# Performance work log

Hardware: AMD Instinct MI355X
Metric: run time of the kernel (lower is better)

The kernel has to match this reference:

```python
import jax, jax.numpy as jnp
import numpy as np

B, C, H, W = 2, 256, 64, 64  # C = in_channels; x has 2*C channels
DQ = C // 16


def setup_inputs() -> dict:
    key = jax.random.key(0)
    ks = jax.random.split(key, 10)
    s = 0.05
    return {
        "x": jax.random.normal(ks[0], (B, 2 * C, H, W), dtype=jnp.float32),
        "Wq": jax.random.normal(ks[1], (DQ, C), dtype=jnp.float32) * s,
        "bq": jax.random.normal(ks[2], (DQ,), dtype=jnp.float32) * s,
        "Wk": jax.random.normal(ks[3], (DQ, C), dtype=jnp.float32) * s,
        "bk": jax.random.normal(ks[4], (DQ,), dtype=jnp.float32) * s,
        "Wv": jax.random.normal(ks[5], (C, C), dtype=jnp.float32) * s,
        "bv": jax.random.normal(ks[6], (C,), dtype=jnp.float32) * s,
        "Wpt": jax.random.normal(ks[7], (C, 2 * C), dtype=jnp.float32) * s,
        "bpt": jax.random.normal(ks[8], (C,), dtype=jnp.float32) * s,
        "gamma": jnp.full((1,), 0.5, dtype=jnp.float32),  # original inits to 0; nonzero for a non-trivial output
    }


def _conv1x1(x, Wt, b):
    # 1x1 conv == per-pixel linear map over channels
    return jnp.einsum("bchw,dc->bdhw", x, Wt) + b[None, :, None, None]


def reference(x, Wq, bq, Wk, bk, Wv, bv, Wpt, bpt, gamma):
    n = x.shape[1] // 2
    x1, x2 = x[:, :n], x[:, n:]
    b, c, h, w = x1.shape
    hw = h * w

    def qkv(xi):
        q = _conv1x1(xi, Wq, bq).reshape(b, DQ, hw)   # [B,dq,HW]
        k = _conv1x1(xi, Wk, bk).reshape(b, DQ, hw)   # [B,dq,HW]
        v = _conv1x1(xi, Wv, bv).reshape(b, c, hw)    # [B,C,HW]
        return q, k, v

    q1, k1, v1 = qkv(x1)
    q2, k2, v2 = qkv(x2)

    # attn[b,i,j] = softmax_j( q[:,i] . k[:,j] )  (no scaling, as in original)
    attn1 = jax.nn.softmax(jnp.einsum("bdi,bdj->bij", q1, k1), axis=-1)  # [B,HW,HW]
    attn2 = jax.nn.softmax(jnp.einsum("bdi,bdj->bij", q2, k2), axis=-1)

    def apply_attn(v, attn):
        # out[b,c,i] = sum_j v[b,c,j] * attn[b,i,j]
        return jnp.einsum("bcj,bij->bci", v, attn).reshape(b, c, h, w)

    out11 = apply_attn(v1, attn1)
    out12 = apply_attn(v2, attn1)
    out21 = apply_attn(v1, attn2)
    out22 = apply_attn(v2, attn2)

    o1 = _conv1x1(jnp.concatenate([out11, out12], axis=1), Wpt, bpt)  # [B,C,H,W]
    o2 = _conv1x1(jnp.concatenate([out21, out22], axis=1), Wpt, bpt)

    out = gamma * jnp.concatenate([o1, o2], axis=1) + x
    return out
```

## Files before the change

### kernel.cpp

```cpp
#include <hip/hip_runtime.h>
#include <hip/hip_bf16.h>


#define HW 4096
#define CC 256
#define DQ 16

typedef __hip_bfloat16 bf16;
struct alignas(8) bh4 { bf16 x, y, z, w; };
typedef __bf16 bf16x8 __attribute__((ext_vector_type(8)));
typedef float  f32x4  __attribute__((ext_vector_type(4)));

static __device__ __forceinline__ float b2f(bf16 v) { return __bfloat162float(v); }

static __device__ __forceinline__ void load_lds16(const void* g, void* l) {
    __builtin_amdgcn_global_load_lds(
        (const __attribute__((address_space(1))) unsigned int*)g,
        (__attribute__((address_space(3))) unsigned int*)l, 16, 0, 0);
}

static __device__ __forceinline__ bf16x8 ones8() {
    union { unsigned int u[4]; bf16x8 v; } t;
    t.u[0] = t.u[1] = t.u[2] = t.u[3] = 0x3F803F80u;
    return t.v;
}

struct ConvArgs { const void* src[9]; float* dst[9]; int n[9]; };
__global__ void convert_weights(ConvArgs a, const unsigned short* __restrict__ probe) {
    int seg = blockIdx.y;
    int i = blockIdx.x * 256 + threadIdx.x;
    bool isb = probe[0] != 0;
    if (i < a.n[seg])
        a.dst[seg][i] = isb ? b2f(((const bf16*)a.src[seg])[i])
                            : ((const float*)a.src[seg])[i];
}

__global__ void w_to_bf16(const float* __restrict__ Wqf, const float* __restrict__ Wkf,
                          bf16* __restrict__ Wqb, bf16* __restrict__ Wkb) {
    int i = blockIdx.x * 256 + threadIdx.x;
    const float* s = blockIdx.y ? Wkf : Wqf;
    bf16* d = blockIdx.y ? Wkb : Wqb;
    d[i] = __float2bfloat16(s[i]);
}

__global__ void convert_x_t(const void* __restrict__ xsrc, bf16* __restrict__ Xt,
                            const unsigned short* __restrict__ probe) {
    __shared__ float T[64][65];
    int t = threadIdx.x;
    int j0 = blockIdx.x * 64, e0 = blockIdx.y * 64, b = blockIdx.z;
    bool isb = probe[0] != 0;
    int j_l = t & 63, er0 = (t >> 6) * 16;
#pragma unroll
    for (int r = 0; r < 16; ++r) {
        size_t src = ((size_t)(b * 512 + e0 + er0 + r)) * HW + j0 + j_l;
        T[er0 + r][j_l] = isb ? b2f(((const bf16*)xsrc)[src]) : ((const float*)xsrc)[src];
    }
    __syncthreads();
    int e_w = t & 63, jr0 = (t >> 6) * 16;
#pragma unroll
    for (int r = 0; r < 16; ++r)
        Xt[((size_t)b * HW + j0 + jr0 + r) * 512 + e0 + e_w] = __float2bfloat16(T[e_w][jr0 + r]);
}

__global__ void build_mc(const float* __restrict__ Wv, const float* __restrict__ bv,
                         const float* __restrict__ Wpt, const float* __restrict__ bpt,
                         bf16* __restrict__ McB, float* __restrict__ btot) {
    int blk = blockIdx.x, tid = threadIdx.x;
    if (blk < 512) {
        int d = blk >> 1;
        int c = ((blk & 1) << 8) + tid;
        int half = c >> 8, cm = c & 255;
        float acc = 0.f;
        for (int e = 0; e < 256; ++e)
            acc = fmaf(Wpt[d * 512 + half * 256 + e], Wv[e * 256 + cm], acc);
        McB[d * 512 + c] = __float2bfloat16(acc);
    } else {
        int d = tid;
        float acc = bpt[d];
        for (int e = 0; e < 256; ++e)
            acc = fmaf(Wpt[d * 512 + e] + Wpt[d * 512 + 256 + e], bv[e], acc);
        btot[d] = acc;
    }
}

__global__ void __launch_bounds__(256)
build_qk_mfma(const bf16* __restrict__ Xt,
              const bf16* __restrict__ Wqb, const float* __restrict__ bqf,
              const bf16* __restrict__ Wkb, const float* __restrict__ bkf,
              bf16* __restrict__ Qb, bf16* __restrict__ Kb) {
    int tid = threadIdx.x;
    int lane = tid & 63, wave = tid >> 6;
    int ln = lane & 15, q = lane >> 4;
    int bh = blockIdx.y;
    int b = bh >> 1, h = bh & 1;
    int j0 = blockIdx.x * 64 + wave * 16;

    bf16x8 aQ[8], aK[8];
#pragma unroll
    for (int kk = 0; kk < 8; ++kk) {
        aQ[kk] = *(const bf16x8*)&Wqb[ln * 256 + kk * 32 + q * 8];
        aK[kk] = *(const bf16x8*)&Wkb[ln * 256 + kk * 32 + q * 8];
    }
    const bf16* Xrow = Xt + ((size_t)b * HW + j0 + ln) * 512 + h * 256;
    f32x4 dQ = {0.f, 0.f, 0.f, 0.f}, dK = {0.f, 0.f, 0.f, 0.f};
#pragma unroll
    for (int kk = 0; kk < 8; ++kk) {
        bf16x8 bx = *(const bf16x8*)&Xrow[kk * 32 + q * 8];
        dQ = __builtin_amdgcn_mfma_f32_16x16x32_bf16(aQ[kk], bx, dQ, 0, 0, 0);
        dK = __builtin_amdgcn_mfma_f32_16x16x32_bf16(aK[kk], bx, dK, 0, 0, 0);
    }
    size_t rowoff = ((size_t)bh * HW + j0 + ln) * 32;
    bh4 oq, ok;
    oq.x = __float2bfloat16(dQ[0] + bqf[q * 4 + 0]);
    oq.y = __float2bfloat16(dQ[1] + bqf[q * 4 + 1]);
    oq.z = __float2bfloat16(dQ[2] + bqf[q * 4 + 2]);
    oq.w = __float2bfloat16(dQ[3] + bqf[q * 4 + 3]);
    ok.x = __float2bfloat16(dK[0] + bkf[q * 4 + 0]);
    ok.y = __float2bfloat16(dK[1] + bkf[q * 4 + 1]);
    ok.z = __float2bfloat16(dK[2] + bkf[q * 4 + 2]);
    ok.w = __float2bfloat16(dK[3] + bkf[q * 4 + 3]);
    bh4 z; z.x = z.y = z.z = z.w = __float2bfloat16(0.f);
    *(bh4*)&Qb[rowoff + q * 4] = oq;
    *(bh4*)&Qb[rowoff + 16 + q * 4] = z;
    *(bh4*)&Kb[rowoff + q * 4] = ok;
    *(bh4*)&Kb[rowoff + 16 + q * 4] = z;
}

__global__ void __launch_bounds__(256, 2)
build_u_mfma(const bf16* __restrict__ McB, const bf16* __restrict__ Xt,
             bf16* __restrict__ Ub) {
    __shared__ __align__(16) bf16 sA[64 * 64];
    __shared__ __align__(16) bf16 sB[128 * 64];
    int tid = threadIdx.x;
    int lane = tid & 63, wave = tid >> 6;
    int ln = lane & 15, q = lane >> 4;
    int wm = (wave >> 1) * 32, wn = (wave & 1) * 64;
    int j0 = blockIdx.x * 128, c0 = blockIdx.y * 64, b = blockIdx.z;
    const bf16* Xb = Xt + (size_t)b * HW * 512;
    f32x4 acc[2][4];
#pragma unroll
    for (int mi = 0; mi < 2; ++mi)
#pragma unroll
        for (int ni = 0; ni < 4; ++ni)
#pragma unroll
            for (int r = 0; r < 4; ++r) acc[mi][ni][r] = 0.f;

    for (int e0 = 0; e0 < 512; e0 += 64) {
        __syncthreads();
#pragma unroll
        for (int r = 0; r < 2; ++r) {
            int s = r * 256 + tid;
            int row = s >> 3, jc = s & 7, jg = jc ^ (row & 7);
            load_lds16(McB + (size_t)(c0 + row) * 512 + e0 + jg * 8, sA + s * 8);
        }
#pragma unroll
        for (int r = 0; r < 4; ++r) {
            int s = r * 256 + tid;
            int row = s >> 3, jc = s & 7, jg = jc ^ (row & 7);
            load_lds16(Xb + (size_t)(j0 + row) * 512 + e0 + jg * 8, sB + s * 8);
        }
        __syncthreads();
#pragma unroll
        for (int kh = 0; kh < 2; ++kh) {
            bf16x8 af[2], bfv[4];
#pragma unroll
            for (int mi = 0; mi < 2; ++mi) {
                int row = wm + mi * 16 + ln;
                int jc = (kh * 4 + q) ^ (row & 7);
                af[mi] = *(const bf16x8*)&sA[row * 64 + jc * 8];
            }
#pragma unroll
            for (int ni = 0; ni < 4; ++ni) {
                int row = wn + ni * 16 + ln;
                int jc = (kh * 4 + q) ^ (row & 7);
                bfv[ni] = *(const bf16x8*)&sB[row * 64 + jc * 8];
            }
#pragma unroll
            for (int mi = 0; mi < 2; ++mi)
#pragma unroll
                for (int ni = 0; ni < 4; ++ni)
                    acc[mi][ni] = __builtin_amdgcn_mfma_f32_16x16x32_bf16(
                        af[mi], bfv[ni], acc[mi][ni], 0, 0, 0);
        }
    }
#pragma unroll
    for (int mi = 0; mi < 2; ++mi)
#pragma unroll
        for (int r = 0; r < 4; ++r) {
            int c = c0 + wm + mi * 16 + q * 4 + r;
#pragma unroll
            for (int ni = 0; ni < 4; ++ni) {
                int j = j0 + wn + ni * 16 + ln;
                Ub[((size_t)(b * CC + c)) * HW + j] = __float2bfloat16(acc[mi][ni][r]);
            }
        }
}

__global__ void __launch_bounds__(256, 4)
compute_E_mfma(const bf16* __restrict__ Qb, const bf16* __restrict__ Kb,
               bf16* __restrict__ E, long estride, int bh_base) {
    int tid = threadIdx.x;
    int lane = tid & 63, wave = tid >> 6;
    int ln = lane & 15, q = lane >> 4;
    int bh = bh_base + blockIdx.z;
    bf16* Eb = E + (size_t)blockIdx.z * estride;
    int i0 = blockIdx.x * 64 + wave * 16;
    int j0 = blockIdx.y * 1024;
    bf16x8 bq = *(const bf16x8*)&Qb[((size_t)bh * HW + i0 + ln) * 32 + q * 8];
    bf16* erow = Eb + (size_t)(i0 + ln) * HW + q * 4;
    for (int jt = 0; jt < 64; ++jt) {
        int j = j0 + jt * 16;
        bf16x8 ak = *(const bf16x8*)&Kb[((size_t)bh * HW + j + ln) * 32 + q * 8];
        f32x4 d = {0.f, 0.f, 0.f, 0.f};
        d = __builtin_amdgcn_mfma_f32_16x16x32_bf16(ak, bq, d, 0, 0, 0);
        bh4 o;
        o.x = __float2bfloat16(__expf(d[0]));
        o.y = __float2bfloat16(__expf(d[1]));
        o.z = __float2bfloat16(__expf(d[2]));
        o.w = __float2bfloat16(__expf(d[3]));
        *(bh4*)&erow[j] = o;
    }
}

__global__ void __launch_bounds__(256, 2)
attn_mfma(const bf16* __restrict__ Ub, const bf16* __restrict__ E, long estride,
          const float* __restrict__ btot,
          const void* __restrict__ xorig, const float* __restrict__ gamf,
          void* __restrict__ outv, const unsigned short* __restrict__ probe,
          int bh_base) {
    __shared__ __align__(16) bf16 sA[128 * 64];
    __shared__ __align__(16) bf16 sB[64 * 64];
    int tid  = threadIdx.x;
    int lane = tid & 63, wave = tid >> 6;
    int ln = lane & 15, q = lane >> 4;
    int wm = (wave & 1) * 64, wn = (wave >> 1) * 32;
    int i0 = blockIdx.x * 64, c0 = blockIdx.y * 128;
    int bh = bh_base + blockIdx.z;
    int b = bh >> 1, h = bh & 1;
    const bf16* Eb = E + (size_t)blockIdx.z * estride;
    const bf16* Ubb = Ub + (size_t)b * CC * HW;
    const bf16x8 ONE = ones8();

    f32x4 acc[4][2], accS[2];
#pragma unroll
    for (int ni = 0; ni < 2; ++ni) {
#pragma unroll
        for (int r = 0; r < 4; ++r) accS[ni][r] = 0.f;
#pragma unroll
        for (int mi = 0; mi < 4; ++mi)
#pragma unroll
            for (int r = 0; r < 4; ++r) acc[mi][ni][r] = 0.f;
    }

    for (int j0 = 0; j0 < HW; j0 += 64) {
        __syncthreads();
#pragma unroll
        for (int r = 0; r < 4; ++r) {
            int s = r * 256 + tid;
            int row = s >> 3, jc = s & 7, jg = jc ^ (row & 7);
            load_lds16(Ubb + (size_t)(c0 + row) * HW + j0 + jg * 8, sA + s * 8);
        }
#pragma unroll
        for (int r = 0; r < 2; ++r) {
            int s = r * 256 + tid;
            int row = s >> 3, jc = s & 7, jg = jc ^ (row & 7);
            load_lds16(Eb + (size_t)(i0 + row) * HW + j0 + jg * 8, sB + s * 8);
        }
        __syncthreads();
#pragma unroll
        for (int kh = 0; kh < 2; ++kh) {
            bf16x8 af[4], bfv[2];
#pragma unroll
            for (int mi = 0; mi < 4; ++mi) {
                int row = wm + mi * 16 + ln;
                int jc = (kh * 4 + q) ^ (row & 7);
                af[mi] = *(const bf16x8*)&sA[row * 64 + jc * 8];
            }
#pragma unroll
            for (int ni = 0; ni < 2; ++ni) {
                int row = wn + ni * 16 + ln;
                int jc = (kh * 4 + q) ^ (row & 7);
                bfv[ni] = *(const bf16x8*)&sB[row * 64 + jc * 8];
            }
#pragma unroll
            for (int ni = 0; ni < 2; ++ni) {
                accS[ni] = __builtin_amdgcn_mfma_f32_16x16x32_bf16(
                    ONE, bfv[ni], accS[ni], 0, 0, 0);
#pragma unroll
                for (int mi = 0; mi < 4; ++mi)
                    acc[mi][ni] = __builtin_amdgcn_mfma_f32_16x16x32_bf16(
                        af[mi], bfv[ni], acc[mi][ni], 0, 0, 0);
            }
        }
    }

    bool isb = probe[0] != 0;
    float g = gamf[0];
    float lv[2];
#pragma unroll
    for (int ni = 0; ni < 2; ++ni)
        lv[ni] = 1.f / accS[ni][0];
#pragma unroll
    for (int mi = 0; mi < 4; ++mi)
#pragma unroll
        for (int r = 0; r < 4; ++r) {
            int c = c0 + wm + mi * 16 + q * 4 + r;
            float bt = btot[c];
            size_t rowbase = ((size_t)(b * 512 + h * 256 + c)) * HW + i0 + wn;
#pragma unroll
            for (int ni = 0; ni < 2; ++ni) {
                size_t idx = rowbase + ni * 16 + ln;
                float xres = isb ? b2f(((const bf16*)xorig)[idx]) : ((const float*)xorig)[idx];
                float o = fmaf(g, fmaf(acc[mi][ni][r], lv[ni], bt), xres);
                if (isb) ((bf16*)outv)[idx] = __float2bfloat16(o);
                else     ((float*)outv)[idx] = o;
            }
        }
}

extern "C" void kernel_launch(void* const* d_in, const int* in_sizes, int n_in,
                              void* d_out, int out_size, void* d_ws, size_t ws_size,
                              hipStream_t stream) {
    const unsigned short* probe = (const unsigned short*)d_in[9];

    char* ws = (char*)d_ws;
    size_t off = 0;
    auto alloc = [&](size_t bytes) { size_t r = off; off = (off + bytes + 255) & ~(size_t)255; return r; };
    const int wsz[9] = {DQ * 256, DQ, DQ * 256, DQ, 256 * 256, 256, 256 * 512, 256, 1};
    float* wf[9];
    for (int t = 0; t < 9; ++t) wf[t] = (float*)(ws + alloc((size_t)wsz[t] * 4));
    bf16*  Xt   = (bf16*)(ws + alloc((size_t)2 * HW * 512 * 2));
    bf16*  McB  = (bf16*)(ws + alloc(256 * 512 * 2));
    float* btot = (float*)(ws + alloc(256 * 4));
    bf16*  Wqb  = (bf16*)(ws + alloc(DQ * 256 * 2));
    bf16*  Wkb  = (bf16*)(ws + alloc(DQ * 256 * 2));
    bf16*  Qb   = (bf16*)(ws + alloc((size_t)4 * HW * 32 * 2));
    bf16*  Kb   = (bf16*)(ws + alloc((size_t)4 * HW * 32 * 2));
    bf16*  Ub   = (bf16*)(ws + alloc((size_t)2 * CC * HW * 2));
    const size_t ESZ = (size_t)HW * HW * 2;
    bf16* E = (bf16*)(ws + off);
    const long ESTRIDE = (long)HW * HW;
    int NZ = (ws_size >= off + 4 * ESZ) ? 4 : 1;

    ConvArgs ca;
    for (int t = 0; t < 9; ++t) { ca.src[t] = d_in[t + 1]; ca.dst[t] = wf[t]; ca.n[t] = wsz[t]; }
    convert_weights<<<dim3(512, 9), 256, 0, stream>>>(ca, probe);
    w_to_bf16<<<dim3(16, 2), 256, 0, stream>>>(wf[0], wf[2], Wqb, Wkb);
    convert_x_t<<<dim3(64, 8, 2), 256, 0, stream>>>(d_in[0], Xt, probe);

    build_mc<<<513, 256, 0, stream>>>(wf[4], wf[5], wf[6], wf[7], McB, btot);
    build_qk_mfma<<<dim3(64, 4), 256, 0, stream>>>(Xt, Wqb, wf[1], Wkb, wf[3], Qb, Kb);
    build_u_mfma<<<dim3(32, 4, 2), 256, 0, stream>>>(McB, Xt, Ub);

    if (NZ == 4) {
        compute_E_mfma<<<dim3(64, 4, 4), 256, 0, stream>>>(Qb, Kb, E, ESTRIDE, 0);
        attn_mfma<<<dim3(64, 2, 4), 256, 0, stream>>>(Ub, E, ESTRIDE, btot, d_in[0], wf[8], d_out, probe, 0);
    } else {
        for (int bh = 0; bh < 4; ++bh) {
            compute_E_mfma<<<dim3(64, 4, 1), 256, 0, stream>>>(Qb, Kb, E, ESTRIDE, bh);
            attn_mfma<<<dim3(64, 2, 1), 256, 0, stream>>>(Ub, E, ESTRIDE, btot, d_in[0], wf[8], d_out, probe, bh);
        }
    }
}
```

Before: 238.9 us.

## Fuse exp-score computation into attention kernel, dropping materialized E matrix

Drops the separate kernel that wrote the full exponentiated score matrix E (4 x 4096 x 4096 bf16) to global memory. The attention kernel now computes each 64x64 tile of exp(QK) on the fly with MFMA and writes it into swizzled LDS, then consumes it as before. This removes a large global write and read-back of E. The cost is that each score tile is recomputed once per channel block (two c-blocks) and the exp work now sits inside the main loop.

```diff
diff --git a/kernel.cpp b/kernel.cpp
--- a/kernel.cpp
+++ b/kernel.cpp
@@ -196,51 +196,26 @@
         }
 }
 
-__global__ void __launch_bounds__(256, 4)
-compute_E_mfma(const bf16* __restrict__ Qb, const bf16* __restrict__ Kb,
-               bf16* __restrict__ E, long estride, int bh_base) {
-    int tid = threadIdx.x;
-    int lane = tid & 63, wave = tid >> 6;
-    int ln = lane & 15, q = lane >> 4;
-    int bh = bh_base + blockIdx.z;
-    bf16* Eb = E + (size_t)blockIdx.z * estride;
-    int i0 = blockIdx.x * 64 + wave * 16;
-    int j0 = blockIdx.y * 1024;
-    bf16x8 bq = *(const bf16x8*)&Qb[((size_t)bh * HW + i0 + ln) * 32 + q * 8];
-    bf16* erow = Eb + (size_t)(i0 + ln) * HW + q * 4;
-    for (int jt = 0; jt < 64; ++jt) {
-        int j = j0 + jt * 16;
-        bf16x8 ak = *(const bf16x8*)&Kb[((size_t)bh * HW + j + ln) * 32 + q * 8];
-        f32x4 d = {0.f, 0.f, 0.f, 0.f};
-        d = __builtin_amdgcn_mfma_f32_16x16x32_bf16(ak, bq, d, 0, 0, 0);
-        bh4 o;
-        o.x = __float2bfloat16(__expf(d[0]));
-        o.y = __float2bfloat16(__expf(d[1]));
-        o.z = __float2bfloat16(__expf(d[2]));
-        o.w = __float2bfloat16(__expf(d[3]));
-        *(bh4*)&erow[j] = o;
-    }
-}
-
 __global__ void __launch_bounds__(256, 2)
-attn_mfma(const bf16* __restrict__ Ub, const bf16* __restrict__ E, long estride,
-          const float* __restrict__ btot,
-          const void* __restrict__ xorig, const float* __restrict__ gamf,
-          void* __restrict__ outv, const unsigned short* __restrict__ probe,
-          int bh_base) {
-    __shared__ __align__(16) bf16 sA[128 * 64];
-    __shared__ __align__(16) bf16 sB[64 * 64];
+flash_attn(const bf16* __restrict__ Ub, const bf16* __restrict__ Qb,
+           const bf16* __restrict__ Kb, const float* __restrict__ btot,
+           const void* __restrict__ xorig, const float* __restrict__ gamf,
+           void* __restrict__ outv, const unsigned short* __restrict__ probe) {
+    __shared__ __align__(16) bf16 sU[128 * 64];
+    __shared__ __align__(16) bf16 sE[64 * 64];
     int tid  = threadIdx.x;
     int lane = tid & 63, wave = tid >> 6;
     int ln = lane & 15, q = lane >> 4;
     int wm = (wave & 1) * 64, wn = (wave >> 1) * 32;
     int i0 = blockIdx.x * 64, c0 = blockIdx.y * 128;
-    int bh = bh_base + blockIdx.z;
+    int bh = blockIdx.z;
     int b = bh >> 1, h = bh & 1;
-    const bf16* Eb = E + (size_t)blockIdx.z * estride;
-    const bf16* Ubb = Ub + (size_t)b * CC * HW;
+    const bf16* Ubb = Ub + (size_t)b * CC * HW + (size_t)c0 * HW;
+    const bf16* Kbh = Kb + (size_t)bh * HW * 32;
     const bf16x8 ONE = ones8();
 
+    bf16x8 bq = *(const bf16x8*)&Qb[((size_t)bh * HW + i0 + wave * 16 + ln) * 32 + q * 8];
+
     f32x4 acc[4][2], accS[2];
 #pragma unroll
     for (int ni = 0; ni < 2; ++ni) {
@@ -251,6 +226,10 @@
 #pragma unroll
             for (int r = 0; r < 4; ++r) acc[mi][ni][r] = 0.f;
     }
+
+    int i_loc = wave * 16 + ln;
+    int wchunk0 = (q >> 1);
+    int woff = (q & 1) * 4;
 
     for (int j0 = 0; j0 < HW; j0 += 64) {
         __syncthreads();
@@ -258,13 +237,20 @@
         for (int r = 0; r < 4; ++r) {
             int s = r * 256 + tid;
             int row = s >> 3, jc = s & 7, jg = jc ^ (row & 7);
-            load_lds16(Ubb + (size_t)(c0 + row) * HW + j0 + jg * 8, sA + s * 8);
-        }
-#pragma unroll
-        for (int r = 0; r < 2; ++r) {
-            int s = r * 256 + tid;
-            int row = s >> 3, jc = s & 7, jg = jc ^ (row & 7);
-            load_lds16(Eb + (size_t)(i0 + row) * HW + j0 + jg * 8, sB + s * 8);
+            load_lds16(Ubb + (size_t)row * HW + j0 + jg * 8, sU + s * 8);
+        }
+#pragma unroll
+        for (int js = 0; js < 4; ++js) {
+            bf16x8 ak = *(const bf16x8*)&Kbh[(size_t)(j0 + js * 16 + ln) * 32 + q * 8];
+            f32x4 d = {0.f, 0.f, 0.f, 0.f};
+            d = __builtin_amdgcn_mfma_f32_16x16x32_bf16(ak, bq, d, 0, 0, 0);
+            bh4 o;
+            o.x = __float2bfloat16(__expf(d[0]));
+            o.y = __float2bfloat16(__expf(d[1]));
+            o.z = __float2bfloat16(__expf(d[2]));
+            o.w = __float2bfloat16(__expf(d[3]));
+            int chunk = (js * 2 + wchunk0) ^ (i_loc & 7);
+            *(bh4*)&sE[i_loc * 64 + chunk * 8 + woff] = o;
         }
         __syncthreads();
 #pragma unroll
@@ -274,13 +260,13 @@
             for (int mi = 0; mi < 4; ++mi) {
                 int row = wm + mi * 16 + ln;
                 int jc = (kh * 4 + q) ^ (row & 7);
-                af[mi] = *(const bf16x8*)&sA[row * 64 + jc * 8];
+                af[mi] = *(const bf16x8*)&sU[row * 64 + jc * 8];
             }
 #pragma unroll
             for (int ni = 0; ni < 2; ++ni) {
                 int row = wn + ni * 16 + ln;
                 int jc = (kh * 4 + q) ^ (row & 7);
-                bfv[ni] = *(const bf16x8*)&sB[row * 64 + jc * 8];
+                bfv[ni] = *(const bf16x8*)&sE[row * 64 + jc * 8];
             }
 #pragma unroll
             for (int ni = 0; ni < 2; ++ni) {
@@ -337,10 +323,6 @@
     bf16*  Qb   = (bf16*)(ws + alloc((size_t)4 * HW * 32 * 2));
     bf16*  Kb   = (bf16*)(ws + alloc((size_t)4 * HW * 32 * 2));
     bf16*  Ub   = (bf16*)(ws + alloc((size_t)2 * CC * HW * 2));
-    const size_t ESZ = (size_t)HW * HW * 2;
-    bf16* E = (bf16*)(ws + off);
-    const long ESTRIDE = (long)HW * HW;
-    int NZ = (ws_size >= off + 4 * ESZ) ? 4 : 1;
 
     ConvArgs ca;
     for (int t = 0; t < 9; ++t) { ca.src[t] = d_in[t + 1]; ca.dst[t] = wf[t]; ca.n[t] = wsz[t]; }
@@ -352,13 +334,5 @@
     build_qk_mfma<<<dim3(64, 4), 256, 0, stream>>>(Xt, Wqb, wf[1], Wkb, wf[3], Qb, Kb);
     build_u_mfma<<<dim3(32, 4, 2), 256, 0, stream>>>(McB, Xt, Ub);
 
-    if (NZ == 4) {
-        compute_E_mfma<<<dim3(64, 4, 4), 256, 0, stream>>>(Qb, Kb, E, ESTRIDE, 0);
-        attn_mfma<<<dim3(64, 2, 4), 256, 0, stream>>>(Ub, E, ESTRIDE, btot, d_in[0], wf[8], d_out, probe, 0);
-    } else {
-        for (int bh = 0; bh < 4; ++bh) {
-            compute_E_mfma<<<dim3(64, 4, 1), 256, 0, stream>>>(Qb, Kb, E, ESTRIDE, bh);
-            attn_mfma<<<dim3(64, 2, 1), 256, 0, stream>>>(Ub, E, ESTRIDE, btot, d_in[0], wf[8], d_out, probe, bh);
-        }
-    }
-}
+    flash_attn<<<dim3(64, 2, 4), 256, 0, stream>>>(Ub, Qb, Kb, btot, d_in[0], wf[8], d_out, probe);
+}
```

New measurement: 207.7 us. 13.1% less time.
